# Kernel tuning notes

Hardware: AMD Instinct MI355X
Metric: run time of the kernel (lower is better)

Reference implementation:

```python
import jax, jax.numpy as jnp
import numpy as np
from jax import lax

NUM_GROUPS = 16
EPS = 1e-5
POOL = 4
CLAMP_MIN, CLAMP_MAX = 0.0, 1.0


def setup_inputs() -> dict:
    key = jax.random.key(0)
    k = jax.random.split(key, 6)
    x = jax.random.normal(k[0], (128, 8, 128, 128), dtype=jnp.float32)
    conv_w = jax.random.normal(k[1], (64, 8, 3, 3), dtype=jnp.float32) * 0.1
    conv_b = jax.random.normal(k[2], (64,), dtype=jnp.float32) * 0.1
    gn_w = jnp.ones((64,), dtype=jnp.float32) + 0.1 * jax.random.normal(k[3], (64,), dtype=jnp.float32)
    gn_b = 0.1 * jax.random.normal(k[4], (64,), dtype=jnp.float32)
    scale = jnp.ones((64, 1, 1), dtype=jnp.float32) + 0.1 * jax.random.normal(k[5], (64, 1, 1), dtype=jnp.float32)
    return {"x": x, "conv_w": conv_w, "conv_b": conv_b, "gn_w": gn_w, "gn_b": gn_b, "scale": scale}


def reference(x, conv_w, conv_b, gn_w, gn_b, scale):
    # Conv2d: stride 1, no padding -> [N, 64, 126, 126]
    y = lax.conv_general_dilated(
        x, conv_w, window_strides=(1, 1), padding="VALID",
        dimension_numbers=("NCHW", "OIHW", "NCHW"))
    y = y + conv_b[None, :, None, None]

    # GroupNorm over (C/G, H, W) per (N, group), biased variance, eps=1e-5
    N, C, H, W = y.shape
    yg = y.reshape(N, NUM_GROUPS, -1)
    mean = jnp.mean(yg, axis=-1, keepdims=True)
    var = jnp.mean(jnp.square(yg - mean), axis=-1, keepdims=True)
    yn = ((yg - mean) * lax.rsqrt(var + EPS)).reshape(N, C, H, W)
    yn = yn * gn_w[None, :, None, None] + gn_b[None, :, None, None]

    # Per-channel scale (scale has shape [C,1,1])
    yn = yn * scale[None]

    # MaxPool2d(kernel=4, stride=4) -> [N, 64, 31, 31]
    yp = lax.reduce_window(yn, -jnp.inf, lax.max,
                           window_dimensions=(1, 1, POOL, POOL),
                           window_strides=(1, 1, POOL, POOL),
                           padding="VALID")

    # Clamp
    return jnp.clip(yp, CLAMP_MIN, CLAMP_MAX)
```

## Files before the change

kernel.cpp:

```cpp
#include <hip/hip_runtime.h>
#include <math.h>

#define N_IMG 128
#define IC 8
#define IH 128
#define IW 128
#define OC 64
#define OH 126
#define OW 126
#define NG 16
#define CPG 4
#define PH 31
#define PW 31
#define GN_EPS 1e-5f

__device__ __forceinline__ void edge2(const float* __restrict__ xb,
                                      const float* wlds_,
                                      int oh, int ow,
                                      float acc[2][CPG]) {
#pragma unroll 1
    for (int ic = 0; ic < IC; ic++) {
        const float* xr = xb + ic * (IH * IW) + oh * IW + ow;
        float xv[3][4];
#pragma unroll
        for (int kh = 0; kh < 3; kh++) {
            float2 a = *(const float2*)(xr + kh * IW);
            float2 b = *(const float2*)(xr + kh * IW + 2);
            xv[kh][0] = a.x; xv[kh][1] = a.y;
            xv[kh][2] = b.x; xv[kh][3] = b.y;
        }
        const float* wk = wlds_ + ic * 36;
#pragma unroll
        for (int kh = 0; kh < 3; kh++) {
            float wr[12];
#pragma unroll
            for (int t = 0; t < 12; t++) wr[t] = wk[kh * 12 + t];
#pragma unroll
            for (int ch = 0; ch < CPG; ch++) {
                float w0 = wr[0 * 4 + ch];
                float w1 = wr[1 * 4 + ch];
                float w2 = wr[2 * 4 + ch];
                acc[0][ch] = fmaf(xv[kh][0], w0,
                             fmaf(xv[kh][1], w1,
                             fmaf(xv[kh][2], w2, acc[0][ch])));
                acc[1][ch] = fmaf(xv[kh][1], w0,
                             fmaf(xv[kh][2], w1,
                             fmaf(xv[kh][3], w2, acc[1][ch])));
            }
        }
    }
}

__device__ __forceinline__ void load6(const float* __restrict__ p,
                                      float (&buf)[6][6]) {
#pragma unroll
    for (int rr = 0; rr < 6; rr++) {
        float4 f4 = *(const float4*)(p + rr * IW);
        float2 f2 = *(const float2*)(p + rr * IW + 4);
        buf[rr][0] = f4.x; buf[rr][1] = f4.y;
        buf[rr][2] = f4.z; buf[rr][3] = f4.w;
        buf[rr][4] = f2.x; buf[rr][5] = f2.y;
    }
}

__device__ __forceinline__ void fma36(const float (&xv)[6][6],
                                      const float* wk,
                                      float (&acc)[4][4][CPG]) {
#pragma unroll
    for (int kh = 0; kh < 3; kh++) {
        float wr[12];
#pragma unroll
        for (int t = 0; t < 12; t++) wr[t] = wk[kh * 12 + t];
#pragma unroll
        for (int ch = 0; ch < CPG; ch++) {
            float w0 = wr[0 * 4 + ch];
            float w1 = wr[1 * 4 + ch];
            float w2 = wr[2 * 4 + ch];
#pragma unroll
            for (int rr = 0; rr < 4; rr++) {
#pragma unroll
                for (int j = 0; j < 4; j++) {
                    acc[rr][j][ch] = fmaf(xv[rr + kh][j],     w0,
                                     fmaf(xv[rr + kh][j + 1], w1,
                                     fmaf(xv[rr + kh][j + 2], w2, acc[rr][j][ch])));
                }
            }
        }
    }
}

__attribute__((amdgpu_waves_per_eu(2, 4)))
__launch_bounds__(256)
__global__ void fused_conv_gn_pool_kernel(const float* __restrict__ x,
                                          const float* __restrict__ conv_w,
                                          const float* __restrict__ conv_b,
                                          const float* __restrict__ gn_w,
                                          const float* __restrict__ gn_b,
                                          const float* __restrict__ scale,
                                          float* __restrict__ out) {
    const int b = blockIdx.x;
    const int wid = ((b & 7) << 8) | (b >> 3);
    const int n = wid >> 4;
    const int g = wid & 15;
    const int tid = threadIdx.x;

    __shared__ float wlds[IC * 3 * 3 * CPG];
    __shared__ float red[8];
    __shared__ float stats[2];

    for (int t = tid; t < IC * 3 * 3 * CPG; t += 256) {
        int ch = t & 3;
        int r = t >> 2;
        int c = g * CPG + ch;
        float sg = (gn_w[c] * scale[c] >= 0.f) ? 1.f : -1.f;
        wlds[t] = conv_w[c * (IC * 9) + r] * sg;
    }
    float biasS[CPG], sgnf[CPG];
#pragma unroll
    for (int ch = 0; ch < CPG; ch++) {
        int c = g * CPG + ch;
        float sg = (gn_w[c] * scale[c] >= 0.f) ? 1.f : -1.f;
        sgnf[ch] = sg;
        biasS[ch] = conv_b[c] * sg;
    }
    __syncthreads();

    const float* xb = x + (size_t)n * (IC * IH * IW);
    const int CS = IH * IW;

    float s_ch[CPG];
    float ss_ch[CPG];
#pragma unroll
    for (int ch = 0; ch < CPG; ch++) { s_ch[ch] = 0.f; ss_ch[ch] = 0.f; }
    float pm[4][CPG];
#pragma unroll
    for (int ci = 0; ci < 4; ci++)
#pragma unroll
        for (int ch = 0; ch < CPG; ch++) pm[ci][ch] = -INFINITY;

#pragma unroll 1
    for (int ci = 0; ci < 4; ci++) {
        int cell = tid + ci * 256;
        if (cell < PH * PW) {
            int ph = cell / PW;
            int pw = cell - ph * PW;
            const int r0 = 4 * ph;
            const float* xcell = xb + r0 * IW + 4 * pw;

            float acc[4][4][CPG];
#pragma unroll
            for (int rr = 0; rr < 4; rr++)
#pragma unroll
                for (int j = 0; j < 4; j++)
#pragma unroll
                    for (int ch = 0; ch < CPG; ch++) acc[rr][j][ch] = biasS[ch];

            float bufA[6][6], bufB[6][6];
            load6(xcell, bufA);

#pragma unroll 1
            for (int ic = 0; ic < IC; ic += 2) {
                load6(xcell + (ic + 1) * CS, bufB);
                fma36(bufA, wlds + ic * 36, acc);
                load6(xcell + ((ic + 2 < IC) ? ic + 2 : ic + 1) * CS, bufA);
                fma36(bufB, wlds + (ic + 1) * 36, acc);
            }

#pragma unroll
            for (int rr = 0; rr < 4; rr++)
#pragma unroll
                for (int j = 0; j < 4; j++)
#pragma unroll
                    for (int ch = 0; ch < CPG; ch++) {
                        float v = acc[rr][j][ch];
                        s_ch[ch] += v;
                        ss_ch[ch] = fmaf(v, v, ss_ch[ch]);
                        pm[ci][ch] = fmaxf(pm[ci][ch], v);
                    }
        }
    }

    if (tid < 250) {
        int oh, ow;
        if (tid < 124) {
            oh = tid; ow = 124;
        } else {
            int u2 = tid - 124;
            int hi = (u2 >= 63) ? 1 : 0;
            oh = 124 + hi;
            ow = (u2 - 63 * hi) * 2;
        }
        float acc[2][CPG];
#pragma unroll
        for (int j = 0; j < 2; j++)
#pragma unroll
            for (int ch = 0; ch < CPG; ch++) acc[j][ch] = biasS[ch];
        edge2(xb, wlds, oh, ow, acc);
#pragma unroll
        for (int j = 0; j < 2; j++)
#pragma unroll
            for (int ch = 0; ch < CPG; ch++) {
                float v = acc[j][ch];
                s_ch[ch] += v;
                ss_ch[ch] = fmaf(v, v, ss_ch[ch]);
            }
    }

    float s = sgnf[0] * s_ch[0] + sgnf[1] * s_ch[1]
            + sgnf[2] * s_ch[2] + sgnf[3] * s_ch[3];
    float ss = ss_ch[0] + ss_ch[1] + ss_ch[2] + ss_ch[3];
#pragma unroll
    for (int off = 32; off > 0; off >>= 1) {
        s  += __shfl_down(s, off, 64);
        ss += __shfl_down(ss, off, 64);
    }
    int wave = tid >> 6;
    if ((tid & 63) == 0) { red[wave] = s; red[4 + wave] = ss; }
    __syncthreads();
    if (tid == 0) {
        float S  = red[0] + red[1] + red[2] + red[3];
        float SS = red[4] + red[5] + red[6] + red[7];
        const float inv_count = 1.f / (float)(CPG * OH * OW);
        float mean = S * inv_count;
        float var = SS * inv_count - mean * mean;
        if (var < 0.f) var = 0.f;
        stats[0] = mean;
        stats[1] = rsqrtf(var + GN_EPS);
    }
    __syncthreads();
    const float mean = stats[0];
    const float rstd = stats[1];

    float a2[CPG], b2[CPG];
#pragma unroll
    for (int ch = 0; ch < CPG; ch++) {
        int c = g * CPG + ch;
        float gw = gn_w[c], sc = scale[c];
        a2[ch] = rstd * fabsf(gw * sc);
        b2[ch] = (gn_b[c] - mean * rstd * gw) * sc;
    }

#pragma unroll
    for (int ci = 0; ci < 4; ci++) {
        int cell = tid + ci * 256;
        if (cell < PH * PW) {
            int ph = cell / PW;
            int pw = cell - ph * PW;
#pragma unroll
            for (int ch = 0; ch < CPG; ch++) {
                int c = g * CPG + ch;
                float v = fmaf(a2[ch], pm[ci][ch], b2[ch]);
                v = fminf(fmaxf(v, 0.f), 1.f);
                out[(((size_t)n * OC + c) * PH + ph) * PW + pw] = v;
            }
        }
    }
}

extern "C" void kernel_launch(void* const* d_in, const int* in_sizes, int n_in,
                              void* d_out, int out_size, void* d_ws, size_t ws_size,
                              hipStream_t stream) {
    const float* x      = (const float*)d_in[0];
    const float* conv_w = (const float*)d_in[1];
    const float* conv_b = (const float*)d_in[2];
    const float* gn_w   = (const float*)d_in[3];
    const float* gn_b   = (const float*)d_in[4];
    const float* scale  = (const float*)d_in[5];
    float* out = (float*)d_out;

    dim3 grid(N_IMG * NG);
    dim3 block(256);
    hipLaunchKernelGGL(fused_conv_gn_pool_kernel, grid, block, 0, stream,
                       x, conv_w, conv_b, gn_w, gn_b, scale, out);
}
```

Before: 313.3 us.

## Split fused kernel into two phases with half-group blocks and separate GN finalize

Each (image, group) block is split into two half blocks that each compute about half of the pooled cells, doubling the grid so the GPU has more parallelism and less tail imbalance. Each half writes its partial sums to workspace and its raw pooled maxima to the output. A second kernel then combines the partial sums, computes GroupNorm stats, and applies the affine, scale and clamp in place. The change also drops the waves_per_eu hint and the double-buffered input loads. In exchange it adds a second launch plus an extra read-modify-write pass over the output, and it relies on the workspace being available.

```diff
diff --git a/kernel.cpp b/kernel.cpp
--- a/kernel.cpp
+++ b/kernel.cpp
@@ -13,6 +13,8 @@
 #define PH 31
 #define PW 31
 #define GN_EPS 1e-5f
+#define CELLS (PH * PW)
+#define HALF0 481
 
 __device__ __forceinline__ void edge2(const float* __restrict__ xb,
                                       const float* wlds_,
@@ -89,24 +91,24 @@
     }
 }
 
-__attribute__((amdgpu_waves_per_eu(2, 4)))
 __launch_bounds__(256)
-__global__ void fused_conv_gn_pool_kernel(const float* __restrict__ x,
-                                          const float* __restrict__ conv_w,
-                                          const float* __restrict__ conv_b,
-                                          const float* __restrict__ gn_w,
-                                          const float* __restrict__ gn_b,
-                                          const float* __restrict__ scale,
-                                          float* __restrict__ out) {
+__global__ void conv_pool_phase1(const float* __restrict__ x,
+                                 const float* __restrict__ conv_w,
+                                 const float* __restrict__ conv_b,
+                                 const float* __restrict__ gn_w,
+                                 const float* __restrict__ gn_b,
+                                 const float* __restrict__ scale,
+                                 float* __restrict__ out,
+                                 float* __restrict__ sums) {
     const int b = blockIdx.x;
-    const int wid = ((b & 7) << 8) | (b >> 3);
-    const int n = wid >> 4;
-    const int g = wid & 15;
+    const int wid = ((b & 7) << 9) | (b >> 3);
+    const int n = wid >> 5;
+    const int g = (wid >> 1) & 15;
+    const int h = wid & 1;
     const int tid = threadIdx.x;
 
     __shared__ float wlds[IC * 3 * 3 * CPG];
     __shared__ float red[8];
-    __shared__ float stats[2];
 
     for (int t = tid; t < IC * 3 * 3 * CPG; t += 256) {
         int ch = t & 3;
@@ -128,20 +130,24 @@
     const float* xb = x + (size_t)n * (IC * IH * IW);
     const int CS = IH * IW;
 
+    const int cbase = h * HALF0;
+    const int ncell = h ? (CELLS - HALF0) : HALF0;
+
     float s_ch[CPG];
     float ss_ch[CPG];
 #pragma unroll
     for (int ch = 0; ch < CPG; ch++) { s_ch[ch] = 0.f; ss_ch[ch] = 0.f; }
-    float pm[4][CPG];
-#pragma unroll
-    for (int ci = 0; ci < 4; ci++)
-#pragma unroll
-        for (int ch = 0; ch < CPG; ch++) pm[ci][ch] = -INFINITY;
-
-#pragma unroll 1
-    for (int ci = 0; ci < 4; ci++) {
-        int cell = tid + ci * 256;
-        if (cell < PH * PW) {
+    float pm[2][CPG];
+#pragma unroll
+    for (int r = 0; r < 2; r++)
+#pragma unroll
+        for (int ch = 0; ch < CPG; ch++) pm[r][ch] = -INFINITY;
+
+#pragma unroll 1
+    for (int r = 0; r < 2; r++) {
+        int slot = r * 256 + tid;
+        if (slot < ncell) {
+            int cell = cbase + slot;
             int ph = cell / PW;
             int pw = cell - ph * PW;
             const int r0 = 4 * ph;
@@ -155,15 +161,11 @@
 #pragma unroll
                     for (int ch = 0; ch < CPG; ch++) acc[rr][j][ch] = biasS[ch];
 
-            float bufA[6][6], bufB[6][6];
-            load6(xcell, bufA);
-
-#pragma unroll 1
-            for (int ic = 0; ic < IC; ic += 2) {
-                load6(xcell + (ic + 1) * CS, bufB);
-                fma36(bufA, wlds + ic * 36, acc);
-                load6(xcell + ((ic + 2 < IC) ? ic + 2 : ic + 1) * CS, bufA);
-                fma36(bufB, wlds + (ic + 1) * 36, acc);
+#pragma unroll 1
+            for (int ic = 0; ic < IC; ic++) {
+                float xv[6][6];
+                load6(xcell + ic * CS, xv);
+                fma36(xv, wlds + ic * 36, acc);
             }
 
 #pragma unroll
@@ -175,17 +177,18 @@
                         float v = acc[rr][j][ch];
                         s_ch[ch] += v;
                         ss_ch[ch] = fmaf(v, v, ss_ch[ch]);
-                        pm[ci][ch] = fmaxf(pm[ci][ch], v);
+                        pm[r][ch] = fmaxf(pm[r][ch], v);
                     }
         }
     }
 
-    if (tid < 250) {
+    if (tid < 125) {
+        int u = h * 125 + tid;
         int oh, ow;
-        if (tid < 124) {
-            oh = tid; ow = 124;
+        if (u < 124) {
+            oh = u; ow = 124;
         } else {
-            int u2 = tid - 124;
+            int u2 = u - 124;
             int hi = (u2 >= 63) ? 1 : 0;
             oh = 124 + hi;
             ow = (u2 - 63 * hi) * 2;
@@ -218,42 +221,52 @@
     if ((tid & 63) == 0) { red[wave] = s; red[4 + wave] = ss; }
     __syncthreads();
     if (tid == 0) {
-        float S  = red[0] + red[1] + red[2] + red[3];
-        float SS = red[4] + red[5] + red[6] + red[7];
-        const float inv_count = 1.f / (float)(CPG * OH * OW);
+        sums[wid * 2]     = red[0] + red[1] + red[2] + red[3];
+        sums[wid * 2 + 1] = red[4] + red[5] + red[6] + red[7];
+    }
+
+#pragma unroll 1
+    for (int r = 0; r < 2; r++) {
+        int slot = r * 256 + tid;
+        if (slot < ncell) {
+            int cell = cbase + slot;
+            int ph = cell / PW;
+            int pw = cell - ph * PW;
+#pragma unroll
+            for (int ch = 0; ch < CPG; ch++) {
+                int c = g * CPG + ch;
+                out[(((size_t)n * OC + c) * PH + ph) * PW + pw] = pm[r][ch];
+            }
+        }
+    }
+}
+
+__launch_bounds__(256)
+__global__ void finalize_phase2(const float* __restrict__ gn_w,
+                                const float* __restrict__ gn_b,
+                                const float* __restrict__ scale,
+                                const float* __restrict__ sums,
+                                float* __restrict__ out) {
+    const int total = N_IMG * OC * CELLS;
+    const float inv_count = 1.f / (float)(CPG * OH * OW);
+    int stride = gridDim.x * 256;
+    for (int i = blockIdx.x * 256 + threadIdx.x; i < total; i += stride) {
+        int n = i / (OC * CELLS);
+        int rem = i - n * (OC * CELLS);
+        int c = rem / CELLS;
+        int g = c >> 2;
+        int wb = (n * 32 + g * 2) * 2;
+        float S  = sums[wb]     + sums[wb + 2];
+        float SS = sums[wb + 1] + sums[wb + 3];
         float mean = S * inv_count;
         float var = SS * inv_count - mean * mean;
         if (var < 0.f) var = 0.f;
-        stats[0] = mean;
-        stats[1] = rsqrtf(var + GN_EPS);
-    }
-    __syncthreads();
-    const float mean = stats[0];
-    const float rstd = stats[1];
-
-    float a2[CPG], b2[CPG];
-#pragma unroll
-    for (int ch = 0; ch < CPG; ch++) {
-        int c = g * CPG + ch;
+        float rstd = rsqrtf(var + GN_EPS);
         float gw = gn_w[c], sc = scale[c];
-        a2[ch] = rstd * fabsf(gw * sc);
-        b2[ch] = (gn_b[c] - mean * rstd * gw) * sc;
-    }
-
-#pragma unroll
-    for (int ci = 0; ci < 4; ci++) {
-        int cell = tid + ci * 256;
-        if (cell < PH * PW) {
-            int ph = cell / PW;
-            int pw = cell - ph * PW;
-#pragma unroll
-            for (int ch = 0; ch < CPG; ch++) {
-                int c = g * CPG + ch;
-                float v = fmaf(a2[ch], pm[ci][ch], b2[ch]);
-                v = fminf(fmaxf(v, 0.f), 1.f);
-                out[(((size_t)n * OC + c) * PH + ph) * PW + pw] = v;
-            }
-        }
+        float a2 = rstd * fabsf(gw * sc);
+        float b2 = (gn_b[c] - mean * rstd * gw) * sc;
+        float v = fmaf(a2, out[i], b2);
+        out[i] = fminf(fmaxf(v, 0.f), 1.f);
     }
 }
 
@@ -267,9 +280,10 @@
     const float* gn_b   = (const float*)d_in[4];
     const float* scale  = (const float*)d_in[5];
     float* out = (float*)d_out;
-
-    dim3 grid(N_IMG * NG);
-    dim3 block(256);
-    hipLaunchKernelGGL(fused_conv_gn_pool_kernel, grid, block, 0, stream,
-                       x, conv_w, conv_b, gn_w, gn_b, scale, out);
-}
+    float* sums = (float*)d_ws;
+
+    hipLaunchKernelGGL(conv_pool_phase1, dim3(N_IMG * NG * 2), dim3(256), 0,
+                       stream, x, conv_w, conv_b, gn_w, gn_b, scale, out, sums);
+    hipLaunchKernelGGL(finalize_phase2, dim3(4096), dim3(256), 0, stream,
+                       gn_w, gn_b, scale, sums, out);
+}
```

Result: slower. 358.5 us (+14.4%).

## Use 512-thread blocks with two cells per thread and drop double-buffered loads

Applied to the files above, without the earlier changes.

Doubles the block size to 512 threads so each thread computes two pooled cells instead of four. The ping-pong input buffering across channel pairs is replaced by a plain per-channel load-then-FMA loop. The waves-per-EU hint is removed and the reduction is widened to eight waves. The aim is to shorten the serial per-thread chain and cut register pressure, relying on more waves to hide memory latency. In exchange it gives up explicit load/compute overlap, and the dynamically indexed pooled-max array in non-unrolled loops may spill to scratch.

```diff
diff --git a/kernel.cpp b/kernel.cpp
--- a/kernel.cpp
+++ b/kernel.cpp
@@ -13,6 +13,7 @@
 #define PH 31
 #define PW 31
 #define GN_EPS 1e-5f
+#define CELLS (PH * PW)
 
 __device__ __forceinline__ void edge2(const float* __restrict__ xb,
                                       const float* wlds_,
@@ -89,8 +90,7 @@
     }
 }
 
-__attribute__((amdgpu_waves_per_eu(2, 4)))
-__launch_bounds__(256)
+__launch_bounds__(512)
 __global__ void fused_conv_gn_pool_kernel(const float* __restrict__ x,
                                           const float* __restrict__ conv_w,
                                           const float* __restrict__ conv_b,
@@ -105,10 +105,10 @@
     const int tid = threadIdx.x;
 
     __shared__ float wlds[IC * 3 * 3 * CPG];
-    __shared__ float red[8];
+    __shared__ float red[16];
     __shared__ float stats[2];
 
-    for (int t = tid; t < IC * 3 * 3 * CPG; t += 256) {
+    for (int t = tid; t < IC * 3 * 3 * CPG; t += 512) {
         int ch = t & 3;
         int r = t >> 2;
         int c = g * CPG + ch;
@@ -132,16 +132,16 @@
     float ss_ch[CPG];
 #pragma unroll
     for (int ch = 0; ch < CPG; ch++) { s_ch[ch] = 0.f; ss_ch[ch] = 0.f; }
-    float pm[4][CPG];
-#pragma unroll
-    for (int ci = 0; ci < 4; ci++)
-#pragma unroll
-        for (int ch = 0; ch < CPG; ch++) pm[ci][ch] = -INFINITY;
-
-#pragma unroll 1
-    for (int ci = 0; ci < 4; ci++) {
-        int cell = tid + ci * 256;
-        if (cell < PH * PW) {
+    float pm[2][CPG];
+#pragma unroll
+    for (int r = 0; r < 2; r++)
+#pragma unroll
+        for (int ch = 0; ch < CPG; ch++) pm[r][ch] = -INFINITY;
+
+#pragma unroll 1
+    for (int r = 0; r < 2; r++) {
+        int cell = r * 512 + tid;
+        if (cell < CELLS) {
             int ph = cell / PW;
             int pw = cell - ph * PW;
             const int r0 = 4 * ph;
@@ -155,15 +155,11 @@
 #pragma unroll
                     for (int ch = 0; ch < CPG; ch++) acc[rr][j][ch] = biasS[ch];
 
-            float bufA[6][6], bufB[6][6];
-            load6(xcell, bufA);
-
-#pragma unroll 1
-            for (int ic = 0; ic < IC; ic += 2) {
-                load6(xcell + (ic + 1) * CS, bufB);
-                fma36(bufA, wlds + ic * 36, acc);
-                load6(xcell + ((ic + 2 < IC) ? ic + 2 : ic + 1) * CS, bufA);
-                fma36(bufB, wlds + (ic + 1) * 36, acc);
+#pragma unroll 1
+            for (int ic = 0; ic < IC; ic++) {
+                float xv[6][6];
+                load6(xcell + ic * CS, xv);
+                fma36(xv, wlds + ic * 36, acc);
             }
 
 #pragma unroll
@@ -175,7 +171,7 @@
                         float v = acc[rr][j][ch];
                         s_ch[ch] += v;
                         ss_ch[ch] = fmaf(v, v, ss_ch[ch]);
-                        pm[ci][ch] = fmaxf(pm[ci][ch], v);
+                        pm[r][ch] = fmaxf(pm[r][ch], v);
                     }
         }
     }
@@ -215,11 +211,12 @@
         ss += __shfl_down(ss, off, 64);
     }
     int wave = tid >> 6;
-    if ((tid & 63) == 0) { red[wave] = s; red[4 + wave] = ss; }
+    if ((tid & 63) == 0) { red[wave] = s; red[8 + wave] = ss; }
     __syncthreads();
     if (tid == 0) {
-        float S  = red[0] + red[1] + red[2] + red[3];
-        float SS = red[4] + red[5] + red[6] + red[7];
+        float S = 0.f, SS = 0.f;
+#pragma unroll
+        for (int w = 0; w < 8; w++) { S += red[w]; SS += red[8 + w]; }
         const float inv_count = 1.f / (float)(CPG * OH * OW);
         float mean = S * inv_count;
         float var = SS * inv_count - mean * mean;
@@ -240,16 +237,16 @@
         b2[ch] = (gn_b[c] - mean * rstd * gw) * sc;
     }
 
-#pragma unroll
-    for (int ci = 0; ci < 4; ci++) {
-        int cell = tid + ci * 256;
-        if (cell < PH * PW) {
+#pragma unroll 1
+    for (int r = 0; r < 2; r++) {
+        int cell = r * 512 + tid;
+        if (cell < CELLS) {
             int ph = cell / PW;
             int pw = cell - ph * PW;
 #pragma unroll
             for (int ch = 0; ch < CPG; ch++) {
                 int c = g * CPG + ch;
-                float v = fmaf(a2[ch], pm[ci][ch], b2[ch]);
+                float v = fmaf(a2[ch], pm[r][ch], b2[ch]);
                 v = fminf(fmaxf(v, 0.f), 1.f);
                 out[(((size_t)n * OC + c) * PH + ph) * PW + pw] = v;
             }
@@ -269,7 +266,7 @@
     float* out = (float*)d_out;
 
     dim3 grid(N_IMG * NG);
-    dim3 block(256);
+    dim3 block(512);
     hipLaunchKernelGGL(fused_conv_gn_pool_kernel, grid, block, 0, stream,
                        x, conv_w, conv_b, gn_w, gn_b, scale, out);
 }
```

Result: slower. 390.9 us (+24.8%).
